# Kernel tuning notes

Measured on AMD Instinct MI355X. Metric: run time of the kernel, lower is better.

Reference implementation:

```python
import jax, jax.numpy as jnp
import numpy as np

N_NODES = 10000
N_EDGES = 320000
D_IN = 256
D_OUT = 256
NEG_SLOPE = 0.2


def setup_inputs() -> dict:
    key = jax.random.key(0)
    ks = jax.random.split(key, 8)
    feature = jax.random.normal(ks[0], (N_NODES, D_IN), dtype=jnp.float32)
    src = jax.random.randint(ks[1], (N_EDGES,), 0, N_NODES, dtype=jnp.int32)
    dst = jax.random.randint(ks[2], (N_EDGES,), 0, N_NODES, dtype=jnp.int32)
    # Xavier-ish scaled weights
    s = 1.0 / np.sqrt(D_IN)
    W_s = jax.random.normal(ks[3], (D_OUT, D_IN), dtype=jnp.float32) * s
    W_t = jax.random.normal(ks[4], (D_OUT, D_IN), dtype=jnp.float32) * s
    W_attn = jax.random.normal(ks[5], (1, D_OUT), dtype=jnp.float32) * (1.0 / np.sqrt(D_OUT))
    W_fc = jax.random.normal(ks[6], (D_OUT, D_IN), dtype=jnp.float32) * s
    b_fc = jnp.zeros((D_OUT,), dtype=jnp.float32)
    return {"feature": feature, "src": src, "dst": dst,
            "W_s": W_s, "W_t": W_t, "W_attn": W_attn,
            "W_fc": W_fc, "b_fc": b_fc}


def reference(feature, src, dst, W_s, W_t, W_attn, W_fc, b_fc):
    n = feature.shape[0]
    # Project at node level, then gather (same math as projecting gathered feats).
    proj_s = feature @ W_s.T          # [N, D_OUT]
    proj_t = feature @ W_t.T          # [N, D_OUT]
    # Edge attention logits: attn(LeakyReLU(h_dst + h_src))
    z = proj_s[src] + proj_t[dst]     # [E, D_OUT]
    z = jnp.where(z >= 0, z, NEG_SLOPE * z)
    e = (z @ W_attn.T)[:, 0]          # [E]
    # edge_softmax with norm_by='src': softmax over outgoing edges of each src node
    m = jax.ops.segment_max(e, src, num_segments=n)          # [N]
    m = jnp.where(jnp.isfinite(m), m, 0.0)                   # guard empty segments
    e_exp = jnp.exp(e - m[src])                               # [E]
    denom = jax.ops.segment_sum(e_exp, src, num_segments=n)  # [N]
    alpha = e_exp / denom[src]                                # [E]
    # message = src feature * alpha; reduce = sum at dst
    msg = feature[src] * alpha[:, None]                       # [E, D_IN]
    agg = jax.ops.segment_sum(msg, dst, num_segments=n)       # [N, D_IN]
    # final linear
    return agg @ W_fc.T + b_fc
```

## Files before the change

kernel.cpp:

```cpp
#include <hip/hip_runtime.h>
#include <math.h>

#define N_NODES 10000
#define N_EDGES 320000
#define D 256
#define NEG_SLOPE 0.2f
#define BCAP 96
#define BLOCK 256
#define NF4 (N_NODES * D / 4)
#define NW4 (256 * 256 / 4)
#define NTILE_M 157
#define NTILES (NTILE_M * 12)
#define FILL_BLOCKS ((N_EDGES + BLOCK - 1) / BLOCK)
#define CPAD 66

typedef unsigned short ushortT;
typedef __attribute__((ext_vector_type(8))) short bf16x8;
typedef __attribute__((ext_vector_type(4))) float f32x4;

__device__ __forceinline__ unsigned short f2bf(float f) {
  unsigned int u = __float_as_uint(f);
  u += 0x7FFFu + ((u >> 16) & 1u);
  return (unsigned short)(u >> 16);
}
__device__ __forceinline__ float bf2f(unsigned short u) {
  return __uint_as_float((unsigned int)u << 16);
}

typedef const __attribute__((address_space(1))) unsigned int* gas_ptr;
typedef __attribute__((address_space(3))) unsigned int* las_ptr;
__device__ __forceinline__ void gload16(const void* g, void* l) {
  __builtin_amdgcn_global_load_lds((gas_ptr)g, (las_ptr)l, 16, 0, 0);
}

__global__ void prep_kernel(const float* __restrict__ feat,
                            const float* __restrict__ Ws,
                            const float* __restrict__ Wt,
                            const float* __restrict__ Wfc,
                            ushortT* __restrict__ featb,
                            ushortT* __restrict__ Wcat,
                            int* __restrict__ cnt,
                            float* __restrict__ denom) {
  const int g = blockIdx.x * blockDim.x + threadIdx.x;
  if (g < NF4) {
    float4 v = ((const float4*)feat)[g];
    ushort4 u;
    u.x = f2bf(v.x); u.y = f2bf(v.y); u.z = f2bf(v.z); u.w = f2bf(v.w);
    ((ushort4*)featb)[g] = u;
    return;
  }
  const int gi = g - NF4;
  if (gi < 3 * NW4) {
    const float* W = (gi < NW4) ? Ws : ((gi < 2 * NW4) ? Wt : Wfc);
    const int off = gi - ((gi < NW4) ? 0 : ((gi < 2 * NW4) ? NW4 : 2 * NW4));
    float4 v = ((const float4*)W)[off];
    ushort4 u;
    u.x = f2bf(v.x); u.y = f2bf(v.y); u.z = f2bf(v.z); u.w = f2bf(v.w);
    ((ushort4*)Wcat)[gi] = u;
    return;
  }
  const int gn = gi - 3 * NW4;
  if (gn < N_NODES) {
    cnt[gn] = 0;
    denom[gn] = 0.f;
  }
}

__global__ __launch_bounds__(256, 2) void proj_fill_kernel(
    const ushortT* __restrict__ featb,
    const ushortT* __restrict__ Wcat,
    const int* __restrict__ src, const int* __restrict__ dst,
    int* __restrict__ cnt, int* __restrict__ src_b,
    ushortT* __restrict__ ps, ushortT* __restrict__ pt,
    ushortT* __restrict__ fcp) {
  __shared__ ushortT Als[64][D];
  __shared__ ushortT Bls[64][D];
  __shared__ ushortT Cls[64][CPAD];

  if (blockIdx.x < FILL_BLOCKS) {
    const int i = blockIdx.x * BLOCK + threadIdx.x;
    if (i < N_EDGES) {
      const int dn = dst[i];
      const int slot = atomicAdd(&cnt[dn], 1);
      if (slot < BCAP) src_b[dn * BCAP + slot] = src[i];
    }
    return;
  }
  const int p = blockIdx.x - FILL_BLOCKS;
  const int m0 = (p / 12) * 64;
  const int by = p % 12;
  ushortT* outp = (by < 4) ? ps : ((by < 8) ? pt : fcp);
  const int col0 = (by & 3) * 64;
  const int n0 = by * 64;

  const int tid = threadIdx.x;
  const int wave = tid >> 6;
  const int lane = tid & 63;
  const int quad = lane >> 4;
  const int l16 = lane & 15;

  const int m_base_t = (wave & 1) * 32;
  const int wn = wave >> 1;

  {
    const int rl = lane >> 5;
    const int cph = lane & 31;
#pragma unroll
    for (int c = 0; c < 8; ++c) {
      const int r = wave * 16 + c * 2 + rl;
      const int clog = cph ^ (r & 7);
      gload16(featb + (size_t)(m0 + r) * D + clog * 8, &Als[wave * 16 + c * 2][0]);
      gload16(Wcat + (size_t)(n0 + r) * D + clog * 8, &Bls[wave * 16 + c * 2][0]);
    }
  }
  __syncthreads();

  f32x4 acc[2][2];
#pragma unroll
  for (int i = 0; i < 2; ++i)
#pragma unroll
    for (int j = 0; j < 2; ++j) acc[i][j] = (f32x4){0.f, 0.f, 0.f, 0.f};

  const int ar0 = m_base_t + l16;
  const int br0 = wn * 32 + l16;
  const int xa = ar0 & 7;
  const int xb = br0 & 7;
#pragma unroll
  for (int kk = 0; kk < 8; ++kk) {
    const int j = kk * 4 + quad;
    const int ea = (j ^ xa) * 8;
    const int eb = (j ^ xb) * 8;
    bf16x8 a0 = *(const bf16x8*)&Als[ar0][ea];
    bf16x8 a1 = *(const bf16x8*)&Als[ar0 + 16][ea];
    bf16x8 b0 = *(const bf16x8*)&Bls[br0][eb];
    bf16x8 b1 = *(const bf16x8*)&Bls[br0 + 16][eb];
    acc[0][0] = __builtin_amdgcn_mfma_f32_16x16x32_bf16(a0, b0, acc[0][0], 0, 0, 0);
    acc[0][1] = __builtin_amdgcn_mfma_f32_16x16x32_bf16(a0, b1, acc[0][1], 0, 0, 0);
    acc[1][0] = __builtin_amdgcn_mfma_f32_16x16x32_bf16(a1, b0, acc[1][0], 0, 0, 0);
    acc[1][1] = __builtin_amdgcn_mfma_f32_16x16x32_bf16(a1, b1, acc[1][1], 0, 0, 0);
  }

#pragma unroll
  for (int mi = 0; mi < 2; ++mi)
#pragma unroll
    for (int r = 0; r < 4; ++r) {
      const int row = m_base_t + mi * 16 + quad * 4 + r;
#pragma unroll
      for (int ni = 0; ni < 2; ++ni)
        Cls[row][wn * 32 + ni * 16 + l16] = f2bf(acc[mi][ni][r]);
    }
  __syncthreads();
#pragma unroll
  for (int it = 0; it < 2; ++it) {
    const int idx = tid + it * 256;
    const int row = idx >> 3;
    const int cc = (idx & 7) * 8;
    const int grow = m0 + row;
    if (grow < N_NODES)
      *(bf16x8*)(outp + (size_t)grow * D + col0 + cc) = *(const bf16x8*)&Cls[row][cc];
  }
}

__global__ __launch_bounds__(256) void logit_bucket_kernel(
    const ushortT* __restrict__ ps,
    const ushortT* __restrict__ pt,
    const int* __restrict__ cnt,
    const int* __restrict__ src_b,
    const float* __restrict__ Wattn,
    float* __restrict__ expv_b,
    float* __restrict__ denom) {
  const int n = blockIdx.x;
  const int cn = min(cnt[n], BCAP);
  if (cn == 0) return;
  const int wave = threadIdx.x >> 6;
  const int lane = threadIdx.x & 63;
  const int half = lane >> 5;
  const int l32 = lane & 31;
  const int grp = wave * 2 + half;
  const int base = n * BCAP;

  bf16x8 bu = *(const bf16x8*)(pt + (size_t)n * D + l32 * 8);
  float b[8], w[8];
  const float4 w0 = *(const float4*)(Wattn + l32 * 8);
  const float4 w1 = *(const float4*)(Wattn + l32 * 8 + 4);
  w[0] = w0.x; w[1] = w0.y; w[2] = w0.z; w[3] = w0.w;
  w[4] = w1.x; w[5] = w1.y; w[6] = w1.z; w[7] = w1.w;
#pragma unroll
  for (int i = 0; i < 8; ++i) b[i] = bf2f((unsigned short)bu[i]);

  int j = grp;
  for (; j + 24 < cn; j += 32) {
    const int s0 = src_b[base + j];
    const int s1 = src_b[base + j + 8];
    const int s2 = src_b[base + j + 16];
    const int s3 = src_b[base + j + 24];
    bf16x8 au0 = *(const bf16x8*)(ps + (size_t)s0 * D + l32 * 8);
    bf16x8 au1 = *(const bf16x8*)(ps + (size_t)s1 * D + l32 * 8);
    bf16x8 au2 = *(const bf16x8*)(ps + (size_t)s2 * D + l32 * 8);
    bf16x8 au3 = *(const bf16x8*)(ps + (size_t)s3 * D + l32 * 8);
    float sum0 = 0.f, sum1 = 0.f, sum2 = 0.f, sum3 = 0.f;
#pragma unroll
    for (int i = 0; i < 8; ++i) {
      float z0 = bf2f((unsigned short)au0[i]) + b[i];
      float z1 = bf2f((unsigned short)au1[i]) + b[i];
      float z2 = bf2f((unsigned short)au2[i]) + b[i];
      float z3 = bf2f((unsigned short)au3[i]) + b[i];
      z0 = fmaxf(z0, NEG_SLOPE * z0);
      z1 = fmaxf(z1, NEG_SLOPE * z1);
      z2 = fmaxf(z2, NEG_SLOPE * z2);
      z3 = fmaxf(z3, NEG_SLOPE * z3);
      sum0 = fmaf(w[i], z0, sum0);
      sum1 = fmaf(w[i], z1, sum1);
      sum2 = fmaf(w[i], z2, sum2);
      sum3 = fmaf(w[i], z3, sum3);
    }
#pragma unroll
    for (int off = 16; off > 0; off >>= 1) {
      sum0 += __shfl_down(sum0, off, 32);
      sum1 += __shfl_down(sum1, off, 32);
      sum2 += __shfl_down(sum2, off, 32);
      sum3 += __shfl_down(sum3, off, 32);
    }
    if (l32 == 0) {
      float ex0 = __expf(sum0), ex1 = __expf(sum1);
      float ex2 = __expf(sum2), ex3 = __expf(sum3);
      expv_b[base + j] = ex0;
      expv_b[base + j + 8] = ex1;
      expv_b[base + j + 16] = ex2;
      expv_b[base + j + 24] = ex3;
      atomicAdd(&denom[s0], ex0);
      atomicAdd(&denom[s1], ex1);
      atomicAdd(&denom[s2], ex2);
      atomicAdd(&denom[s3], ex3);
    }
  }
  for (; j < cn; j += 8) {
    const int s = src_b[base + j];
    bf16x8 au = *(const bf16x8*)(ps + (size_t)s * D + l32 * 8);
    float sum = 0.f;
#pragma unroll
    for (int i = 0; i < 8; ++i) {
      float z = bf2f((unsigned short)au[i]) + b[i];
      z = fmaxf(z, NEG_SLOPE * z);
      sum = fmaf(w[i], z, sum);
    }
#pragma unroll
    for (int off = 16; off > 0; off >>= 1) sum += __shfl_down(sum, off, 32);
    if (l32 == 0) {
      float ex = __expf(sum);
      expv_b[base + j] = ex;
      atomicAdd(&denom[s], ex);
    }
  }
}

__global__ __launch_bounds__(256) void gather_agg_kernel(
    const ushortT* __restrict__ fcp,
    const int* __restrict__ cnt,
    const int* __restrict__ src_b,
    const float* __restrict__ expv_b,
    const float* __restrict__ denom,
    const float* __restrict__ b_fc,
    float* __restrict__ out) {
  __shared__ float red[8][D];
  const int n = blockIdx.x;
  const int tid = threadIdx.x;
  const int wave = tid >> 6;
  const int lane = tid & 63;
  const int half = lane >> 5;
  const int l32 = lane & 31;
  const int grp = wave * 2 + half;
  const int cn = min(cnt[n], BCAP);
  const int base = n * BCAP;

  float acc[8];
#pragma unroll
  for (int i = 0; i < 8; ++i) acc[i] = 0.f;

  int j = grp;
  for (; j + 24 < cn; j += 32) {
    const int s0 = src_b[base + j];
    const int s1 = src_b[base + j + 8];
    const int s2 = src_b[base + j + 16];
    const int s3 = src_b[base + j + 24];
    const float a0 = expv_b[base + j] / denom[s0];
    const float a1 = expv_b[base + j + 8] / denom[s1];
    const float a2 = expv_b[base + j + 16] / denom[s2];
    const float a3 = expv_b[base + j + 24] / denom[s3];
    bf16x8 f0 = *(const bf16x8*)(fcp + (size_t)s0 * D + l32 * 8);
    bf16x8 f1 = *(const bf16x8*)(fcp + (size_t)s1 * D + l32 * 8);
    bf16x8 f2 = *(const bf16x8*)(fcp + (size_t)s2 * D + l32 * 8);
    bf16x8 f3 = *(const bf16x8*)(fcp + (size_t)s3 * D + l32 * 8);
#pragma unroll
    for (int i = 0; i < 8; ++i) {
      acc[i] = fmaf(a0, bf2f((unsigned short)f0[i]), acc[i]);
      acc[i] = fmaf(a1, bf2f((unsigned short)f1[i]), acc[i]);
      acc[i] = fmaf(a2, bf2f((unsigned short)f2[i]), acc[i]);
      acc[i] = fmaf(a3, bf2f((unsigned short)f3[i]), acc[i]);
    }
  }
  for (; j < cn; j += 8) {
    const int s = src_b[base + j];
    const float a = expv_b[base + j] / denom[s];
    bf16x8 fu = *(const bf16x8*)(fcp + (size_t)s * D + l32 * 8);
#pragma unroll
    for (int i = 0; i < 8; ++i)
      acc[i] = fmaf(a, bf2f((unsigned short)fu[i]), acc[i]);
  }
  *(float4*)&red[grp][l32 * 8] = make_float4(acc[0], acc[1], acc[2], acc[3]);
  *(float4*)&red[grp][l32 * 8 + 4] = make_float4(acc[4], acc[5], acc[6], acc[7]);
  __syncthreads();
  float o = b_fc[tid];
#pragma unroll
  for (int g = 0; g < 8; ++g) o += red[g][tid];
  out[(size_t)n * D + tid] = o;
}

extern "C" void kernel_launch(void* const* d_in, const int* in_sizes, int n_in,
                              void* d_out, int out_size, void* d_ws, size_t ws_size,
                              hipStream_t stream) {
  const float* feat  = (const float*)d_in[0];
  const int*   src   = (const int*)d_in[1];
  const int*   dst   = (const int*)d_in[2];
  const float* Ws    = (const float*)d_in[3];
  const float* Wt    = (const float*)d_in[4];
  const float* Wattn = (const float*)d_in[5];
  const float* Wfc   = (const float*)d_in[6];
  const float* bfc   = (const float*)d_in[7];
  float* out = (float*)d_out;

  ushortT* ps    = (ushortT*)d_ws;
  ushortT* pt    = ps + (size_t)N_NODES * D;
  ushortT* fcp   = pt + (size_t)N_NODES * D;
  ushortT* featb = fcp + (size_t)N_NODES * D;
  ushortT* Wcat  = featb + (size_t)N_NODES * D;
  float* expv_b  = (float*)(Wcat + (size_t)768 * 256);
  float* denom   = expv_b + (size_t)N_NODES * BCAP;
  int*   cnt     = (int*)(denom + N_NODES);
  int*   src_b   = cnt + N_NODES;

  const int prep_items = NF4 + 3 * NW4 + N_NODES;
  prep_kernel<<<(prep_items + BLOCK - 1) / BLOCK, BLOCK, 0, stream>>>(
      feat, Ws, Wt, Wfc, featb, Wcat, cnt, denom);
  proj_fill_kernel<<<FILL_BLOCKS + NTILES, BLOCK, 0, stream>>>(
      featb, Wcat, src, dst, cnt, src_b, ps, pt, fcp);
  logit_bucket_kernel<<<N_NODES, BLOCK, 0, stream>>>(ps, pt, cnt, src_b, Wattn, expv_b, denom);
  gather_agg_kernel<<<N_NODES, BLOCK, 0, stream>>>(fcp, cnt, src_b, expv_b, denom, bfc, out);
}
```

Baseline: 162.5 us.

## Map one wave per destination node in logit and aggregation kernels

```diff
diff --git a/kernel.cpp b/kernel.cpp
--- a/kernel.cpp
+++ b/kernel.cpp
@@ -169,14 +169,14 @@
     const float* __restrict__ Wattn,
     float* __restrict__ expv_b,
     float* __restrict__ denom) {
-  const int n = blockIdx.x;
+  const int wave = threadIdx.x >> 6;
+  const int n = blockIdx.x * 4 + wave;
+  if (n >= N_NODES) return;
   const int cn = min(cnt[n], BCAP);
   if (cn == 0) return;
-  const int wave = threadIdx.x >> 6;
   const int lane = threadIdx.x & 63;
   const int half = lane >> 5;
   const int l32 = lane & 31;
-  const int grp = wave * 2 + half;
   const int base = n * BCAP;
 
   bf16x8 bu = *(const bf16x8*)(pt + (size_t)n * D + l32 * 8);
@@ -188,12 +188,12 @@
 #pragma unroll
   for (int i = 0; i < 8; ++i) b[i] = bf2f((unsigned short)bu[i]);
 
-  int j = grp;
-  for (; j + 24 < cn; j += 32) {
+  int j = half;
+  for (; j + 6 < cn; j += 8) {
     const int s0 = src_b[base + j];
-    const int s1 = src_b[base + j + 8];
-    const int s2 = src_b[base + j + 16];
-    const int s3 = src_b[base + j + 24];
+    const int s1 = src_b[base + j + 2];
+    const int s2 = src_b[base + j + 4];
+    const int s3 = src_b[base + j + 6];
     bf16x8 au0 = *(const bf16x8*)(ps + (size_t)s0 * D + l32 * 8);
     bf16x8 au1 = *(const bf16x8*)(ps + (size_t)s1 * D + l32 * 8);
     bf16x8 au2 = *(const bf16x8*)(ps + (size_t)s2 * D + l32 * 8);
@@ -225,16 +225,16 @@
       float ex0 = __expf(sum0), ex1 = __expf(sum1);
       float ex2 = __expf(sum2), ex3 = __expf(sum3);
       expv_b[base + j] = ex0;
-      expv_b[base + j + 8] = ex1;
-      expv_b[base + j + 16] = ex2;
-      expv_b[base + j + 24] = ex3;
+      expv_b[base + j + 2] = ex1;
+      expv_b[base + j + 4] = ex2;
+      expv_b[base + j + 6] = ex3;
       atomicAdd(&denom[s0], ex0);
       atomicAdd(&denom[s1], ex1);
       atomicAdd(&denom[s2], ex2);
       atomicAdd(&denom[s3], ex3);
     }
   }
-  for (; j < cn; j += 8) {
+  for (; j < cn; j += 2) {
     const int s = src_b[base + j];
     bf16x8 au = *(const bf16x8*)(ps + (size_t)s * D + l32 * 8);
     float sum = 0.f;
@@ -262,14 +262,12 @@
     const float* __restrict__ denom,
     const float* __restrict__ b_fc,
     float* __restrict__ out) {
-  __shared__ float red[8][D];
-  const int n = blockIdx.x;
-  const int tid = threadIdx.x;
-  const int wave = tid >> 6;
-  const int lane = tid & 63;
+  const int wave = threadIdx.x >> 6;
+  const int n = blockIdx.x * 4 + wave;
+  if (n >= N_NODES) return;
+  const int lane = threadIdx.x & 63;
   const int half = lane >> 5;
   const int l32 = lane & 31;
-  const int grp = wave * 2 + half;
   const int cn = min(cnt[n], BCAP);
   const int base = n * BCAP;
 
@@ -277,16 +275,16 @@
 #pragma unroll
   for (int i = 0; i < 8; ++i) acc[i] = 0.f;
 
-  int j = grp;
-  for (; j + 24 < cn; j += 32) {
+  int j = half;
+  for (; j + 6 < cn; j += 8) {
     const int s0 = src_b[base + j];
-    const int s1 = src_b[base + j + 8];
-    const int s2 = src_b[base + j + 16];
-    const int s3 = src_b[base + j + 24];
+    const int s1 = src_b[base + j + 2];
+    const int s2 = src_b[base + j + 4];
+    const int s3 = src_b[base + j + 6];
     const float a0 = expv_b[base + j] / denom[s0];
-    const float a1 = expv_b[base + j + 8] / denom[s1];
-    const float a2 = expv_b[base + j + 16] / denom[s2];
-    const float a3 = expv_b[base + j + 24] / denom[s3];
+    const float a1 = expv_b[base + j + 2] / denom[s1];
+    const float a2 = expv_b[base + j + 4] / denom[s2];
+    const float a3 = expv_b[base + j + 6] / denom[s3];
     bf16x8 f0 = *(const bf16x8*)(fcp + (size_t)s0 * D + l32 * 8);
     bf16x8 f1 = *(const bf16x8*)(fcp + (size_t)s1 * D + l32 * 8);
     bf16x8 f2 = *(const bf16x8*)(fcp + (size_t)s2 * D + l32 * 8);
@@ -299,7 +297,7 @@
       acc[i] = fmaf(a3, bf2f((unsigned short)f3[i]), acc[i]);
     }
   }
-  for (; j < cn; j += 8) {
+  for (; j < cn; j += 2) {
     const int s = src_b[base + j];
     const float a = expv_b[base + j] / denom[s];
     bf16x8 fu = *(const bf16x8*)(fcp + (size_t)s * D + l32 * 8);
@@ -307,13 +305,16 @@
     for (int i = 0; i < 8; ++i)
       acc[i] = fmaf(a, bf2f((unsigned short)fu[i]), acc[i]);
   }
-  *(float4*)&red[grp][l32 * 8] = make_float4(acc[0], acc[1], acc[2], acc[3]);
-  *(float4*)&red[grp][l32 * 8 + 4] = make_float4(acc[4], acc[5], acc[6], acc[7]);
-  __syncthreads();
-  float o = b_fc[tid];
-#pragma unroll
-  for (int g = 0; g < 8; ++g) o += red[g][tid];
-  out[(size_t)n * D + tid] = o;
+#pragma unroll
+  for (int i = 0; i < 8; ++i) acc[i] += __shfl_xor(acc[i], 32);
+  if (half == 0) {
+    const float4 bf0 = *(const float4*)(b_fc + l32 * 8);
+    const float4 bf1 = *(const float4*)(b_fc + l32 * 8 + 4);
+    float4 o0 = make_float4(acc[0] + bf0.x, acc[1] + bf0.y, acc[2] + bf0.z, acc[3] + bf0.w);
+    float4 o1 = make_float4(acc[4] + bf1.x, acc[5] + bf1.y, acc[6] + bf1.z, acc[7] + bf1.w);
+    *(float4*)(out + (size_t)n * D + l32 * 8) = o0;
+    *(float4*)(out + (size_t)n * D + l32 * 8 + 4) = o1;
+  }
 }
 
 extern "C" void kernel_launch(void* const* d_in, const int* in_sizes, int n_in,
@@ -340,10 +341,11 @@
   int*   src_b   = cnt + N_NODES;
 
   const int prep_items = NF4 + 3 * NW4 + N_NODES;
+  const int nodeblocks = (N_NODES + 3) / 4;
   prep_kernel<<<(prep_items + BLOCK - 1) / BLOCK, BLOCK, 0, stream>>>(
       feat, Ws, Wt, Wfc, featb, Wcat, cnt, denom);
   proj_fill_kernel<<<FILL_BLOCKS + NTILES, BLOCK, 0, stream>>>(
       featb, Wcat, src, dst, cnt, src_b, ps, pt, fcp);
-  logit_bucket_kernel<<<N_NODES, BLOCK, 0, stream>>>(ps, pt, cnt, src_b, Wattn, expv_b, denom);
-  gather_agg_kernel<<<N_NODES, BLOCK, 0, stream>>>(fcp, cnt, src_b, expv_b, denom, bfc, out);
-}
+  logit_bucket_kernel<<<nodeblocks, BLOCK, 0, stream>>>(ps, pt, cnt, src_b, Wattn, expv_b, denom);
+  gather_agg_kernel<<<nodeblocks, BLOCK, 0, stream>>>(fcp, cnt, src_b, expv_b, denom, bfc, out);
+}
```

After: 162.1 us. Within noise of the previous version (-0.3%).
